# Kernel tuning notes

Hardware: AMD Instinct MI355X
Metric: run time of the kernel (lower is better)

The kernel has to match this reference:

```python
import jax, jax.numpy as jnp
import numpy as np
import math

# BDH config (defaults from BDHConfig)
D = 256        # n_embd
NH = 4         # n_head
MULT = 128     # mlp_internal_dim_multiplier
N = MULT * D // NH   # 8192 latent dim per head
NLAYER = 6
VOCAB = 256
B, T = 1, 1024
THETA = 2.0 ** 16
TWO_PI = 2.0 * math.pi


def _freqs(n):
    # get_freqs: quantize exponent to even integers
    t = jnp.arange(n, dtype=jnp.float32)
    q = jnp.floor(t / 2.0) * 2.0
    return 1.0 / (THETA ** (q / n)) / TWO_PI  # [N]


def _ln(x, eps=1e-5):
    # LayerNorm without affine params (elementwise_affine=False)
    m = jnp.mean(x, axis=-1, keepdims=True)
    v = jnp.mean((x - m) ** 2, axis=-1, keepdims=True)
    return (x - m) / jnp.sqrt(v + eps)


def _rope(phases, v):
    # phases: [T,N] broadcastable to v [...,T,N]
    ph = (phases % 1.0) * TWO_PI
    cos, sin = jnp.cos(ph), jnp.sin(ph)
    # rotate adjacent pairs: (-v_odd, v_even) interleaved
    vrot = jnp.stack((-v[..., 1::2], v[..., ::2]), axis=-1).reshape(v.shape)
    return v * cos + vrot * sin


def setup_inputs() -> dict:
    key = jax.random.key(0)
    ks = jax.random.split(key, 6)
    std = 0.02
    return {
        "idx": jax.random.randint(ks[0], (B, T), 0, VOCAB),
        "embed_w": jax.random.normal(ks[1], (VOCAB, D), jnp.float32) * std,
        "encoder": jax.random.normal(ks[2], (NH, D, N), jnp.float32) * std,
        "encoder_v": jax.random.normal(ks[3], (NH, D, N), jnp.float32) * std,
        "decoder": jax.random.normal(ks[4], (NH * N, D), jnp.float32) * std,
        "lm_head": jax.random.normal(ks[5], (D, VOCAB), jnp.float32) * std,
    }


def reference(idx, embed_w, encoder, encoder_v, decoder, lm_head):
    freqs = _freqs(N)                                             # [N]
    phases = jnp.arange(T, dtype=jnp.float32)[:, None] * freqs    # [T,N]
    mask = jnp.tril(jnp.ones((T, T), jnp.float32), k=-1)          # strict causal
    dec = decoder.reshape(NH, N, D)

    x = _ln(embed_w[idx])                                         # [B,T,D]
    for _ in range(NLAYER):
        x_sp = jax.nn.relu(jnp.einsum('btd,hdn->bhtn', x, encoder))   # [B,nh,T,N]
        qr = _rope(phases, x_sp)                                       # [B,nh,T,N]
        scores = jnp.einsum('bhtn,bhsn->bhts', qr, qr) * mask          # [B,nh,T,T]
        ykv = _ln(jnp.einsum('bhts,bsd->bhtd', scores, x))             # [B,nh,T,D]
        y_sp = jax.nn.relu(jnp.einsum('bhtd,hdn->bhtn', ykv, encoder_v))
        xy = x_sp * y_sp                                               # [B,nh,T,N]
        ymlp = jnp.einsum('bhtn,hnd->btd', xy, dec)                    # [B,T,D]
        x = _ln(x + _ln(ymlp))
    return x @ lm_head                                                 # [B,T,VOCAB]
```

## Files before the change

kernel.cpp:

```cpp
#include <hip/hip_runtime.h>
#include <hip/hip_bf16.h>
#include <math.h>

#define T_ 1024
#define D_ 256
#define N_ 8192
#define NH_ 4
#define NLAYER_ 6
#define VOCAB_ 256
#define TWO_PI_F 6.283185307179586f
#define INV_TWO_PI_F 0.15915494309189535f

#define SC_HSTR32 294912u
#define SC_SSTR32 1179648u
#define SC_SPLIT_BYTES 4718592u
#define SC_NSPLIT 8

typedef __attribute__((ext_vector_type(8))) short short8;
typedef __attribute__((ext_vector_type(4))) float floatx4;
typedef unsigned short ushort_t;

__device__ __forceinline__ void cp16(const void* g, void* l) {
    __builtin_amdgcn_global_load_lds((const __attribute__((address_space(1))) unsigned int*)g,
                                     (__attribute__((address_space(3))) unsigned int*)l,
                                     16, 0, 0);
}

__device__ __forceinline__ float bf2f_raw(unsigned short u) {
    union { unsigned int i; float f; } x;
    x.i = ((unsigned int)u) << 16;
    return x.f;
}
__device__ __forceinline__ unsigned int f2bf_u(float f) {
    union { float f; unsigned int u; } x; x.f = f;
    return (x.u + 0x7fffu + ((x.u >> 16) & 1u)) >> 16;
}
__device__ __forceinline__ float fsin_rev(float ph) {
    float r; asm("v_sin_f32 %0, %1" : "=v"(r) : "v"(ph)); return r;
}
__device__ __forceinline__ float fcos_rev(float ph) {
    float r; asm("v_cos_f32 %0, %1" : "=v"(r) : "v"(ph)); return r;
}

__device__ __forceinline__ float block_sum(float v, float* red) {
    #pragma unroll
    for (int s = 32; s > 0; s >>= 1) v += __shfl_xor(v, s);
    int tid = threadIdx.x;
    if ((tid & 63) == 0) red[tid >> 6] = v;
    __syncthreads();
    float r = red[0] + red[1] + red[2] + red[3];
    __syncthreads();
    return r;
}


__global__ void k_embed_ln(const int* __restrict__ idx, const float* __restrict__ ew,
                           float* __restrict__ x, __hip_bfloat16* __restrict__ x_bf) {
    __shared__ float red[4];
    int t = blockIdx.x, d = threadIdx.x;
    float v = ew[idx[t] * D_ + d];
    float mean = block_sum(v, red) * (1.0f / D_);
    float c = v - mean;
    float var = block_sum(c * c, red) * (1.0f / D_);
    float o = c * rsqrtf(var + 1e-5f);
    x[t * D_ + d] = o;
    x_bf[t * D_ + d] = __float2bfloat16(o);
}

__global__ void k_ln_rows(const float* __restrict__ yp, __hip_bfloat16* __restrict__ outb) {
    __shared__ float red[4];
    int r = blockIdx.x, d = threadIdx.x;
    const size_t S = (size_t)NH_ * T_ * D_;
    float v = yp[(size_t)r * D_ + d] + yp[S + (size_t)r * D_ + d];
    float mean = block_sum(v, red) * (1.0f / D_);
    float c = v - mean;
    float var = block_sum(c * c, red) * (1.0f / D_);
    outb[(size_t)r * D_ + d] = __float2bfloat16(c * rsqrtf(var + 1e-5f));
}

__global__ void k_x_update(float* __restrict__ x, const float* __restrict__ ypart,
                           __hip_bfloat16* __restrict__ x_bf) {
    __shared__ float red[4];
    int t = blockIdx.x, d = threadIdx.x;
    float v = 0.0f;
    #pragma unroll
    for (int i = 0; i < 32; i++) v += ypart[(size_t)i * T_ * D_ + t * D_ + d];
    float m1 = block_sum(v, red) * (1.0f / D_);
    float c1 = v - m1;
    float v1 = block_sum(c1 * c1, red) * (1.0f / D_);
    float u = c1 * rsqrtf(v1 + 1e-5f);
    float w = x[t * D_ + d] + u;
    float m2 = block_sum(w, red) * (1.0f / D_);
    float c2 = w - m2;
    float v2 = block_sum(c2 * c2, red) * (1.0f / D_);
    float o = c2 * rsqrtf(v2 + 1e-5f);
    x[t * D_ + d] = o;
    x_bf[t * D_ + d] = __float2bfloat16(o);
}

__global__ __launch_bounds__(256) void k_tcvt(const float* __restrict__ in,
                                              __hip_bfloat16* __restrict__ out,
                                              int R, int C) {
    int h = blockIdx.z;
    int r0 = blockIdx.y * 32, c0 = blockIdx.x * 32;
    __shared__ float tile[32][33];
    int tx = threadIdx.x & 31, ty = threadIdx.x >> 5;
    const float* inh = in + (size_t)h * R * C;
    __hip_bfloat16* outh = out + (size_t)h * R * C;
    #pragma unroll
    for (int i = 0; i < 4; i++)
        tile[ty + 8 * i][tx] = inh[(size_t)(r0 + ty + 8 * i) * C + c0 + tx];
    __syncthreads();
    #pragma unroll
    for (int i = 0; i < 4; i++)
        outh[(size_t)(c0 + ty + 8 * i) * R + r0 + tx] = __float2bfloat16(tile[tx][ty + 8 * i]);
}

__device__ __forceinline__ void gemm128(const ushort_t* __restrict__ A,
                                        const ushort_t* __restrict__ B,
                                        int lda, int ldb, int K,
                                        ushort_t* As, ushort_t* Bs,
                                        floatx4 acc[4][4]) {
    const int tid = threadIdx.x;
    const int lane = tid & 63, wid = tid >> 6;
    const int wm = wid >> 1, wn = wid & 1;
    const int quad = lane >> 4, col = lane & 15;
    int srow[4], scol[4];
    #pragma unroll
    for (int i = 0; i < 4; i++) {
        int s = i * 256 + tid;
        srow[i] = s >> 3;
        scol[i] = (s & 7) ^ (srow[i] & 7);
    }
    for (int k0 = 0; k0 < K; k0 += 64) {
        #pragma unroll
        for (int i = 0; i < 4; i++)
            cp16(A + (size_t)srow[i] * lda + k0 + scol[i] * 8,
                 As + (size_t)(i * 256 + wid * 64) * 8);
        #pragma unroll
        for (int i = 0; i < 4; i++)
            cp16(B + (size_t)srow[i] * ldb + k0 + scol[i] * 8,
                 Bs + (size_t)(i * 256 + wid * 64) * 8);
        __syncthreads();
        #pragma unroll
        for (int kk = 0; kk < 2; kk++) {
            short8 af[4], bf[4];
            #pragma unroll
            for (int mi = 0; mi < 4; mi++) {
                int row = wm * 64 + mi * 16 + col;
                int pc = ((kk << 2) + quad) ^ (row & 7);
                af[mi] = *(const short8*)&As[row * 64 + pc * 8];
            }
            #pragma unroll
            for (int ni = 0; ni < 4; ni++) {
                int row = wn * 64 + ni * 16 + col;
                int pc = ((kk << 2) + quad) ^ (row & 7);
                bf[ni] = *(const short8*)&Bs[row * 64 + pc * 8];
            }
            #pragma unroll
            for (int mi = 0; mi < 4; mi++)
                #pragma unroll
                for (int ni = 0; ni < 4; ni++)
                    acc[mi][ni] = __builtin_amdgcn_mfma_f32_16x16x32_bf16(
                        af[mi], bf[ni], acc[mi][ni], 0, 0, 0);
        }
        __syncthreads();
    }
}

#define GEMM_PROLOGUE()                                              \
    __shared__ __align__(16) ushort_t smem[2 * 128 * 64];            \
    ushort_t* As = smem;                                             \
    ushort_t* Bs = smem + 128 * 64;                                  \
    floatx4 acc[4][4];                                               \
    _Pragma("unroll") for (int mi = 0; mi < 4; mi++)                 \
        _Pragma("unroll") for (int ni = 0; ni < 4; ni++)             \
            acc[mi][ni] = (floatx4){0.f, 0.f, 0.f, 0.f};             \
    const int lane = threadIdx.x & 63, wid = threadIdx.x >> 6;       \
    const int wm = wid >> 1, wn = wid & 1;                           \
    const int quad = lane >> 4, col = lane & 15;                     \
    const int odd = lane & 1;                                        \
    const int rsel = odd ? 2 : 0, rother = odd ? 0 : 2;

__global__ __launch_bounds__(256) void k_scores_m(const __hip_bfloat16* __restrict__ qr,
                                                  __hip_bfloat16* __restrict__ scp) {
    const int b = blockIdx.x;
    const int slice = b & 31;
    const int h = slice & 3, ks = slice >> 2;
    int i = b >> 5;
    int ti = 0;
    while ((ti + 1) * (ti + 2) / 2 <= i) ti++;
    int si = i - ti * (ti + 1) / 2;
    const int t0 = ti * 128, s0 = si * 128;
    GEMM_PROLOGUE();
    const ushort_t* qh = (const ushort_t*)qr + (size_t)h * T_ * N_ + (size_t)ks * (N_ / 8);
    gemm128(qh + (size_t)t0 * N_, qh + (size_t)s0 * N_, N_, N_, N_ / 8, As, Bs, acc);
    unsigned int* osm = (unsigned int*)smem;
    #pragma unroll
    for (int mi = 0; mi < 4; mi++)
        #pragma unroll
        for (int ni = 0; ni < 4; ni++) {
            const int ss = s0 + wn * 64 + ni * 16 + col;
            const int cc = (wn * 64 + ni * 16 + col) >> 1;
            const int rowb = wm * 64 + mi * 16 + quad * 4;
            #pragma unroll
            for (int rr = 0; rr < 2; rr++) {
                int tt_o = rowb + rother + rr;
                float send = (ss < t0 + tt_o) ? acc[mi][ni][rother + rr] : 0.0f;
                float recv = __shfl_xor(send, 1);
                int tt = rowb + rsel + rr;
                float mine = (ss < t0 + tt) ? acc[mi][ni][rsel + rr] : 0.0f;
                float lo = odd ? recv : mine, hi = odd ? mine : recv;
                osm[tt * 64 + (cc ^ ((tt & 7) << 3))] = f2bf_u(lo) | (f2bf_u(hi) << 16);
            }
        }
    __syncthreads();
    const unsigned int Wu = (unsigned int)(ti + 1) * 64;
    unsigned int* bb = (unsigned int*)scp + (size_t)ks * SC_SSTR32 + (size_t)h * SC_HSTR32
                       + (size_t)4096 * ti * (ti + 1);
    uint4* sc4 = (uint4*)bb;
    const uint4* osm4 = (const uint4*)osm;
    #pragma unroll
    for (int i2 = 0; i2 < 8; i2++) {
        int idx = i2 * 256 + threadIdx.x;
        int row = idx >> 4, c4 = idx & 15;
        uint4 w = osm4[row * 16 + (c4 ^ ((row & 7) << 1))];
        sc4[((size_t)row * Wu + (size_t)si * 64) / 4 + c4] = w;
    }
}

__global__ void k_sc_cvt(__hip_bfloat16* __restrict__ scp) {
    const uint4* __restrict__ sp4 = (const uint4*)scp;
    uint4* sp4o = (uint4*)scp;
    int b = blockIdx.x;
    int head = b & 3;
    unsigned int t4 = (unsigned int)(b >> 2) * 256u + threadIdx.x;
    size_t off = (size_t)head * (SC_HSTR32 / 4) + t4;
    float a0 = 0.f, a1 = 0.f, a2 = 0.f, a3 = 0.f, a4 = 0.f, a5 = 0.f, a6 = 0.f, a7 = 0.f;
    #pragma unroll
    for (int s = 0; s < SC_NSPLIT; s++) {
        uint4 w = sp4[off + (size_t)s * (SC_SSTR32 / 4)];
        a0 += bf2f_raw((unsigned short)(w.x & 0xffff));
        a1 += bf2f_raw((unsigned short)(w.x >> 16));
        a2 += bf2f_raw((unsigned short)(w.y & 0xffff));
        a3 += bf2f_raw((unsigned short)(w.y >> 16));
        a4 += bf2f_raw((unsigned short)(w.z & 0xffff));
        a5 += bf2f_raw((unsigned short)(w.z >> 16));
        a6 += bf2f_raw((unsigned short)(w.w & 0xffff));
        a7 += bf2f_raw((unsigned short)(w.w >> 16));
    }
    uint4 o;
    o.x = f2bf_u(a0) | (f2bf_u(a1) << 16);
    o.y = f2bf_u(a2) | (f2bf_u(a3) << 16);
    o.z = f2bf_u(a4) | (f2bf_u(a5) << 16);
    o.w = f2bf_u(a6) | (f2bf_u(a7) << 16);
    sp4o[off] = o;
}

template <int MODE>
__global__ __launch_bounds__(256) void k_proj_m(const __hip_bfloat16* __restrict__ Abf,
                                                const __hip_bfloat16* __restrict__ Wt,
                                                __hip_bfloat16* __restrict__ out1) {
    const int h = blockIdx.z;
    const int t0 = blockIdx.y * 128, n0 = blockIdx.x * 128;
    GEMM_PROLOGUE();
    const ushort_t* Ah = (const ushort_t*)Abf + (MODE ? (size_t)h * T_ * D_ : (size_t)0)
                         + (size_t)t0 * D_;
    const ushort_t* Bh = (const ushort_t*)Wt + (size_t)h * N_ * D_ + (size_t)n0 * D_;
    gemm128(Ah, Bh, D_, D_, D_, As, Bs, acc);
    unsigned int* osm = (unsigned int*)smem;
    unsigned int xw[4][4][2];
    if (MODE == 1) {
        const unsigned int* q32 = (const unsigned int*)out1;
        const int c4p = lane & 15, rl4 = lane >> 4;
        #pragma unroll
        for (int i = 0; i < 8; i++) {
            int chunk = i * 4 + wid;
            int row_l = chunk * 4 + rl4;
            size_t g32 = (size_t)(h * T_ + t0 + row_l) * (size_t)(N_ / 2) + (size_t)(n0 >> 1)
                         + (size_t)(4 * (c4p ^ ((row_l & 7) << 1)));
            cp16(q32 + g32, osm + chunk * 256);
        }
        __syncthreads();
        #pragma unroll
        for (int ni = 0; ni < 4; ni++) {
            const int cc = (wn * 64 + ni * 16 + col) >> 1;
            #pragma unroll
            for (int mi = 0; mi < 4; mi++) {
                const int rowb = wm * 64 + mi * 16 + quad * 4;
                #pragma unroll
                for (int rr = 0; rr < 2; rr++) {
                    int tt = rowb + rsel + rr;
                    xw[ni][mi][rr] = osm[tt * 64 + (cc ^ ((tt & 7) << 3))];
                }
            }
        }
        __syncthreads();
    }
    #pragma unroll
    for (int ni = 0; ni < 4; ni++) {
        const int cc = (wn * 64 + ni * 16 + col) >> 1;
        const int nn_e = (n0 + wn * 64 + ni * 16 + col) & ~1;
        const float freq = exp2f((float)(nn_e >> 1) * (-1.0f / 256.0f)) * INV_TWO_PI_F;
        #pragma unroll
        for (int mi = 0; mi < 4; mi++) {
            const int rowb = wm * 64 + mi * 16 + quad * 4;
            #pragma unroll
            for (int rr = 0; rr < 2; rr++) {
                float send = fmaxf(acc[mi][ni][rother + rr], 0.0f);
                float recv = __shfl_xor(send, 1);
                float mine = fmaxf(acc[mi][ni][rsel + rr], 0.0f);
                float ve = odd ? recv : mine, vo = odd ? mine : recv;
                int tt = rowb + rsel + rr;
                float ph = (float)(t0 + tt) * freq;
                ph -= floorf(ph);
                float c = fcos_rev(ph), s = fsin_rev(ph);
                unsigned int pk;
                if (MODE == 0) {
                    pk = f2bf_u(ve * c - vo * s) | (f2bf_u(vo * c + ve * s) << 16);
                } else {
                    unsigned int w = xw[ni][mi][rr];
                    float qe = bf2f_raw((unsigned short)(w & 0xffff));
                    float qo = bf2f_raw((unsigned short)(w >> 16));
                    pk = f2bf_u(ve * (qe * c + qo * s)) | (f2bf_u(vo * (qo * c - qe * s)) << 16);
                }
                osm[tt * 64 + (cc ^ ((tt & 7) << 3))] = pk;
            }
        }
    }
    __syncthreads();
    uint4* o4 = (uint4*)out1;
    const uint4* osm4 = (const uint4*)osm;
    #pragma unroll
    for (int i2 = 0; i2 < 8; i2++) {
        int idx = i2 * 256 + threadIdx.x;
        int row = idx >> 4, c4 = idx & 15;
        uint4 w = osm4[row * 16 + (c4 ^ ((row & 7) << 1))];
        o4[(size_t)(h * T_ + t0 + row) * (size_t)(N_ / 8) + (size_t)(n0 >> 3) + c4] = w;
    }
}

__global__ __launch_bounds__(256) void k_ykv_m(const __hip_bfloat16* __restrict__ sc,
                                               const __hip_bfloat16* __restrict__ xT,
                                               float* __restrict__ ykvp) {
    const int b = blockIdx.x;
    const int h = (b >> 1) & 3, ks = b & 1;
    const int r0 = b >> 3;
    const int d0 = (r0 & 1) * 128, t0 = (r0 >> 1) * 128;
    GEMM_PROLOGUE();
    const int W = t0 + 128;
    const int half = W >> 1;
    const int ti = t0 >> 7;
    const ushort_t* Ah = (const ushort_t*)sc + (size_t)h * 589824u
                         + (size_t)8192 * ti * (ti + 1) + (size_t)ks * half;
    const ushort_t* Bh = (const ushort_t*)xT + (size_t)d0 * T_ + (size_t)ks * half;
    gemm128(Ah, Bh, W, T_, half, As, Bs, acc);
    float2* yp = (float2*)(ykvp + (size_t)ks * NH_ * T_ * D_);
    #pragma unroll
    for (int mi = 0; mi < 4; mi++)
        #pragma unroll
        for (int ni = 0; ni < 4; ni++) {
            const int dd_e = (d0 + wn * 64 + ni * 16 + col) & ~1;
            const int rowb = t0 + wm * 64 + mi * 16 + quad * 4;
            #pragma unroll
            for (int rr = 0; rr < 2; rr++) {
                float send = acc[mi][ni][rother + rr];
                float recv = __shfl_xor(send, 1);
                float mine = acc[mi][ni][rsel + rr];
                int tt = rowb + rsel + rr;
                yp[(((size_t)h * T_ + tt) * D_ + dd_e) >> 1] =
                    odd ? make_float2(recv, mine) : make_float2(mine, recv);
            }
        }
}

__global__ __launch_bounds__(256) void k_ymlp_m(const __hip_bfloat16* __restrict__ xy,
                                                const __hip_bfloat16* __restrict__ decT,
                                                float* __restrict__ ypart) {
    const int b = blockIdx.x;
    const int slice = b & 31;
    const int ks = slice >> 2, h = slice & 3;
    const int r0 = b >> 5;
    const int d0 = (r0 & 1) * 128, t0 = (r0 >> 1) * 128;
    GEMM_PROLOGUE();
    const ushort_t* Ah = (const ushort_t*)xy + (size_t)h * T_ * N_ + (size_t)t0 * N_ + ks * 1024;
    const ushort_t* Bh = (const ushort_t*)decT + (size_t)h * D_ * N_ + (size_t)d0 * N_ + ks * 1024;
    gemm128(Ah, Bh, N_, N_, 1024, As, Bs, acc);
    float2* yp = (float2*)(ypart + (size_t)slice * T_ * D_);
    #pragma unroll
    for (int mi = 0; mi < 4; mi++)
        #pragma unroll
        for (int ni = 0; ni < 4; ni++) {
            const int dd_e = (d0 + wn * 64 + ni * 16 + col) & ~1;
            const int rowb = t0 + wm * 64 + mi * 16 + quad * 4;
            #pragma unroll
            for (int rr = 0; rr < 2; rr++) {
                float send = acc[mi][ni][rother + rr];
                float recv = __shfl_xor(send, 1);
                float mine = acc[mi][ni][rsel + rr];
                int tt = rowb + rsel + rr;
                yp[((size_t)tt * D_ + dd_e) >> 1] =
                    odd ? make_float2(recv, mine) : make_float2(mine, recv);
            }
        }
}

__global__ __launch_bounds__(256) void k_lmhead_m(const __hip_bfloat16* __restrict__ x_bf,
                                                  const __hip_bfloat16* __restrict__ lmT,
                                                  float* __restrict__ out) {
    const int v0 = blockIdx.x * 128, t0 = blockIdx.y * 128;
    GEMM_PROLOGUE();
    const ushort_t* Ah = (const ushort_t*)x_bf + (size_t)t0 * D_;
    const ushort_t* Bh = (const ushort_t*)lmT + (size_t)v0 * D_;
    gemm128(Ah, Bh, D_, D_, D_, As, Bs, acc);
    float2* op = (float2*)out;
    #pragma unroll
    for (int mi = 0; mi < 4; mi++)
        #pragma unroll
        for (int ni = 0; ni < 4; ni++) {
            const int vv_e = (v0 + wn * 64 + ni * 16 + col) & ~1;
            const int rowb = t0 + wm * 64 + mi * 16 + quad * 4;
            #pragma unroll
            for (int rr = 0; rr < 2; rr++) {
                float send = acc[mi][ni][rother + rr];
                float recv = __shfl_xor(send, 1);
                float mine = acc[mi][ni][rsel + rr];
                int tt = rowb + rsel + rr;
                op[((size_t)tt * VOCAB_ + vv_e) >> 1] =
                    odd ? make_float2(recv, mine) : make_float2(mine, recv);
            }
        }
}


extern "C" void kernel_launch(void* const* d_in, const int* in_sizes, int n_in,
                              void* d_out, int out_size, void* d_ws, size_t ws_size,
                              hipStream_t stream) {
    const int* idx = (const int*)d_in[0];
    const float* embed_w = (const float*)d_in[1];
    const float* encoder = (const float*)d_in[2];
    const float* encoder_v = (const float*)d_in[3];
    const float* decoder = (const float*)d_in[4];
    const float* lm_head = (const float*)d_in[5];
    float* out = (float*)d_out;

    char* p = (char*)d_ws;
    auto alloc = [&](size_t bytes) {
        char* q = p;
        p += (bytes + 255) & ~(size_t)255;
        return q;
    };
    float* x = (float*)alloc((size_t)T_ * D_ * 4);
    __hip_bfloat16* x_bf = (__hip_bfloat16*)alloc((size_t)T_ * D_ * 2);
    __hip_bfloat16* xT = (__hip_bfloat16*)alloc((size_t)T_ * D_ * 2);
    __hip_bfloat16* ykv_bf = (__hip_bfloat16*)alloc((size_t)NH_ * T_ * D_ * 2);
    __hip_bfloat16* scp = (__hip_bfloat16*)alloc((size_t)SC_NSPLIT * SC_SPLIT_BYTES);
    __hip_bfloat16* qr = (__hip_bfloat16*)alloc((size_t)NH_ * T_ * N_ * 2);
    __hip_bfloat16* encT = (__hip_bfloat16*)alloc((size_t)NH_ * N_ * D_ * 2);
    __hip_bfloat16* encvT = (__hip_bfloat16*)alloc((size_t)NH_ * N_ * D_ * 2);
    __hip_bfloat16* decT = (__hip_bfloat16*)alloc((size_t)NH_ * N_ * D_ * 2);
    __hip_bfloat16* lmT = (__hip_bfloat16*)alloc((size_t)VOCAB_ * D_ * 2);
    float* ypart = (float*)alloc((size_t)32 * T_ * D_ * 4);
    float* ykvp = (float*)((char*)scp + SC_SPLIT_BYTES);

    k_tcvt<<<dim3(N_ / 32, D_ / 32, NH_), 256, 0, stream>>>(encoder, encT, D_, N_);
    k_tcvt<<<dim3(N_ / 32, D_ / 32, NH_), 256, 0, stream>>>(encoder_v, encvT, D_, N_);
    k_tcvt<<<dim3(D_ / 32, N_ / 32, NH_), 256, 0, stream>>>(decoder, decT, N_, D_);
    k_tcvt<<<dim3(VOCAB_ / 32, D_ / 32, 1), 256, 0, stream>>>(lm_head, lmT, D_, VOCAB_);

    k_embed_ln<<<T_, 256, 0, stream>>>(idx, embed_w, x, x_bf);
    for (int l = 0; l < NLAYER_; l++) {
        k_proj_m<0><<<dim3(N_ / 128, T_ / 128, NH_), 256, 0, stream>>>(x_bf, encT, qr);
        k_scores_m<<<36 * 32, 256, 0, stream>>>(qr, scp);
        k_sc_cvt<<<1152, 256, 0, stream>>>(scp);
        k_tcvt<<<dim3(D_ / 32, T_ / 32, 1), 256, 0, stream>>>(x, xT, T_, D_);
        k_ykv_m<<<16 * 8, 256, 0, stream>>>(scp, xT, ykvp);
        k_ln_rows<<<NH_ * T_, 256, 0, stream>>>(ykvp, ykv_bf);
        k_proj_m<1><<<dim3(N_ / 128, T_ / 128, NH_), 256, 0, stream>>>(ykv_bf, encvT, qr );
        k_ymlp_m<<<16 * 32, 256, 0, stream>>>(qr, decT, ypart);
        k_x_update<<<T_, 256, 0, stream>>>(x, ypart, x_bf);
    }
    k_lmhead_m<<<dim3(VOCAB_ / 128, T_ / 128), 256, 0, stream>>>(x_bf, lmT, out);
}
```

Before: 1.306 ms.

## Widen projection tiles to 128x256 and split ykv K-range four ways

The projection GEMM now computes a 128x256 output tile per block with its own inline MFMA loop, reusing each loaded A tile across twice as many columns. The RoPE/gating epilogue runs in two 128-column halves. The ykv kernel splits the causal K range into four balanced chunks instead of two, doubling the block count. The row LayerNorm now sums four partial buffers. The trade-off is higher register and LDS pressure in the projection kernel, which may lower occupancy, plus extra partial-sum traffic for ykv.

```diff
diff --git a/kernel.cpp b/kernel.cpp
--- a/kernel.cpp
+++ b/kernel.cpp
@@ -71,7 +71,9 @@
     __shared__ float red[4];
     int r = blockIdx.x, d = threadIdx.x;
     const size_t S = (size_t)NH_ * T_ * D_;
-    float v = yp[(size_t)r * D_ + d] + yp[S + (size_t)r * D_ + d];
+    float v = 0.0f;
+    #pragma unroll
+    for (int s = 0; s < 4; s++) v += yp[(size_t)s * S + (size_t)r * D_ + d];
     float mean = block_sum(v, red) * (1.0f / D_);
     float c = v - mean;
     float var = block_sum(c * c, red) * (1.0f / D_);
@@ -262,81 +264,142 @@
                                                 const __hip_bfloat16* __restrict__ Wt,
                                                 __hip_bfloat16* __restrict__ out1) {
     const int h = blockIdx.z;
-    const int t0 = blockIdx.y * 128, n0 = blockIdx.x * 128;
-    GEMM_PROLOGUE();
+    const int t0 = blockIdx.y * 128, n0 = blockIdx.x * 256;
+    __shared__ __align__(16) ushort_t smem[(128 + 256) * 64];
+    ushort_t* As = smem;
+    ushort_t* Bs = smem + 128 * 64;
+    floatx4 acc[4][8];
+    #pragma unroll
+    for (int mi = 0; mi < 4; mi++)
+        #pragma unroll
+        for (int nj = 0; nj < 8; nj++) acc[mi][nj] = (floatx4){0.f, 0.f, 0.f, 0.f};
+    const int tid = threadIdx.x;
+    const int lane = tid & 63, wid = tid >> 6;
+    const int wm = wid >> 1, wn = wid & 1;
+    const int quad = lane >> 4, col = lane & 15;
+    const int odd = lane & 1;
+    const int rsel = odd ? 2 : 0, rother = odd ? 0 : 2;
     const ushort_t* Ah = (const ushort_t*)Abf + (MODE ? (size_t)h * T_ * D_ : (size_t)0)
                          + (size_t)t0 * D_;
     const ushort_t* Bh = (const ushort_t*)Wt + (size_t)h * N_ * D_ + (size_t)n0 * D_;
-    gemm128(Ah, Bh, D_, D_, D_, As, Bs, acc);
+    int srA[4], scA[4], srB[8], scB[8];
+    #pragma unroll
+    for (int i = 0; i < 4; i++) {
+        int s = i * 256 + tid;
+        srA[i] = s >> 3; scA[i] = (s & 7) ^ (srA[i] & 7);
+    }
+    #pragma unroll
+    for (int i = 0; i < 8; i++) {
+        int s = i * 256 + tid;
+        srB[i] = s >> 3; scB[i] = (s & 7) ^ (srB[i] & 7);
+    }
+    for (int k0 = 0; k0 < D_; k0 += 64) {
+        #pragma unroll
+        for (int i = 0; i < 4; i++)
+            cp16(Ah + (size_t)srA[i] * D_ + k0 + scA[i] * 8, As + (i * 256 + wid * 64) * 8);
+        #pragma unroll
+        for (int i = 0; i < 8; i++)
+            cp16(Bh + (size_t)srB[i] * D_ + k0 + scB[i] * 8, Bs + (i * 256 + wid * 64) * 8);
+        __syncthreads();
+        #pragma unroll
+        for (int kk = 0; kk < 2; kk++) {
+            short8 af[4], bfv[8];
+            #pragma unroll
+            for (int mi = 0; mi < 4; mi++) {
+                int row = wm * 64 + mi * 16 + col;
+                int pc = ((kk << 2) + quad) ^ (row & 7);
+                af[mi] = *(const short8*)&As[row * 64 + pc * 8];
+            }
+            #pragma unroll
+            for (int nj = 0; nj < 8; nj++) {
+                int row = (nj >> 2) * 128 + wn * 64 + (nj & 3) * 16 + col;
+                int pc = ((kk << 2) + quad) ^ (row & 7);
+                bfv[nj] = *(const short8*)&Bs[row * 64 + pc * 8];
+            }
+            #pragma unroll
+            for (int mi = 0; mi < 4; mi++)
+                #pragma unroll
+                for (int nj = 0; nj < 8; nj++)
+                    acc[mi][nj] = __builtin_amdgcn_mfma_f32_16x16x32_bf16(
+                        af[mi], bfv[nj], acc[mi][nj], 0, 0, 0);
+        }
+        __syncthreads();
+    }
     unsigned int* osm = (unsigned int*)smem;
-    unsigned int xw[4][4][2];
-    if (MODE == 1) {
-        const unsigned int* q32 = (const unsigned int*)out1;
-        const int c4p = lane & 15, rl4 = lane >> 4;
-        #pragma unroll
-        for (int i = 0; i < 8; i++) {
-            int chunk = i * 4 + wid;
-            int row_l = chunk * 4 + rl4;
-            size_t g32 = (size_t)(h * T_ + t0 + row_l) * (size_t)(N_ / 2) + (size_t)(n0 >> 1)
-                         + (size_t)(4 * (c4p ^ ((row_l & 7) << 1)));
-            cp16(q32 + g32, osm + chunk * 256);
+    #pragma unroll
+    for (int h2 = 0; h2 < 2; h2++) {
+        unsigned int xw[4][4][2];
+        if (MODE == 1) {
+            const unsigned int* q32 = (const unsigned int*)out1;
+            const int c4p = lane & 15, rl4 = lane >> 4;
+            #pragma unroll
+            for (int i = 0; i < 8; i++) {
+                int chunk = i * 4 + wid;
+                int row_l = chunk * 4 + rl4;
+                size_t g32 = (size_t)(h * T_ + t0 + row_l) * (size_t)(N_ / 2)
+                             + (size_t)((n0 + h2 * 128) >> 1)
+                             + (size_t)(4 * (c4p ^ ((row_l & 7) << 1)));
+                cp16(q32 + g32, osm + chunk * 256);
+            }
+            __syncthreads();
+            #pragma unroll
+            for (int ni = 0; ni < 4; ni++) {
+                const int cc = (wn * 64 + ni * 16 + col) >> 1;
+                #pragma unroll
+                for (int mi = 0; mi < 4; mi++) {
+                    const int rowb = wm * 64 + mi * 16 + quad * 4;
+                    #pragma unroll
+                    for (int rr = 0; rr < 2; rr++) {
+                        int tt = rowb + rsel + rr;
+                        xw[ni][mi][rr] = osm[tt * 64 + (cc ^ ((tt & 7) << 3))];
+                    }
+                }
+            }
         }
         __syncthreads();
         #pragma unroll
         for (int ni = 0; ni < 4; ni++) {
             const int cc = (wn * 64 + ni * 16 + col) >> 1;
+            const int nn_e = (n0 + h2 * 128 + wn * 64 + ni * 16 + col) & ~1;
+            const float freq = exp2f((float)(nn_e >> 1) * (-1.0f / 256.0f)) * INV_TWO_PI_F;
             #pragma unroll
             for (int mi = 0; mi < 4; mi++) {
                 const int rowb = wm * 64 + mi * 16 + quad * 4;
                 #pragma unroll
                 for (int rr = 0; rr < 2; rr++) {
+                    float send = fmaxf(acc[mi][h2 * 4 + ni][rother + rr], 0.0f);
+                    float recv = __shfl_xor(send, 1);
+                    float mine = fmaxf(acc[mi][h2 * 4 + ni][rsel + rr], 0.0f);
+                    float ve = odd ? recv : mine, vo = odd ? mine : recv;
                     int tt = rowb + rsel + rr;
-                    xw[ni][mi][rr] = osm[tt * 64 + (cc ^ ((tt & 7) << 3))];
+                    float ph = (float)(t0 + tt) * freq;
+                    ph -= floorf(ph);
+                    float c = fcos_rev(ph), s = fsin_rev(ph);
+                    unsigned int pk;
+                    if (MODE == 0) {
+                        pk = f2bf_u(ve * c - vo * s) | (f2bf_u(vo * c + ve * s) << 16);
+                    } else {
+                        unsigned int w = xw[ni][mi][rr];
+                        float qe = bf2f_raw((unsigned short)(w & 0xffff));
+                        float qo = bf2f_raw((unsigned short)(w >> 16));
+                        pk = f2bf_u(ve * (qe * c + qo * s)) | (f2bf_u(vo * (qo * c - qe * s)) << 16);
+                    }
+                    osm[tt * 64 + (cc ^ ((tt & 7) << 3))] = pk;
                 }
             }
         }
         __syncthreads();
-    }
-    #pragma unroll
-    for (int ni = 0; ni < 4; ni++) {
-        const int cc = (wn * 64 + ni * 16 + col) >> 1;
-        const int nn_e = (n0 + wn * 64 + ni * 16 + col) & ~1;
-        const float freq = exp2f((float)(nn_e >> 1) * (-1.0f / 256.0f)) * INV_TWO_PI_F;
-        #pragma unroll
-        for (int mi = 0; mi < 4; mi++) {
-            const int rowb = wm * 64 + mi * 16 + quad * 4;
-            #pragma unroll
-            for (int rr = 0; rr < 2; rr++) {
-                float send = fmaxf(acc[mi][ni][rother + rr], 0.0f);
-                float recv = __shfl_xor(send, 1);
-                float mine = fmaxf(acc[mi][ni][rsel + rr], 0.0f);
-                float ve = odd ? recv : mine, vo = odd ? mine : recv;
-                int tt = rowb + rsel + rr;
-                float ph = (float)(t0 + tt) * freq;
-                ph -= floorf(ph);
-                float c = fcos_rev(ph), s = fsin_rev(ph);
-                unsigned int pk;
-                if (MODE == 0) {
-                    pk = f2bf_u(ve * c - vo * s) | (f2bf_u(vo * c + ve * s) << 16);
-                } else {
-                    unsigned int w = xw[ni][mi][rr];
-                    float qe = bf2f_raw((unsigned short)(w & 0xffff));
-                    float qo = bf2f_raw((unsigned short)(w >> 16));
-                    pk = f2bf_u(ve * (qe * c + qo * s)) | (f2bf_u(vo * (qo * c - qe * s)) << 16);
-                }
-                osm[tt * 64 + (cc ^ ((tt & 7) << 3))] = pk;
-            }
-        }
-    }
-    __syncthreads();
-    uint4* o4 = (uint4*)out1;
-    const uint4* osm4 = (const uint4*)osm;
-    #pragma unroll
-    for (int i2 = 0; i2 < 8; i2++) {
-        int idx = i2 * 256 + threadIdx.x;
-        int row = idx >> 4, c4 = idx & 15;
-        uint4 w = osm4[row * 16 + (c4 ^ ((row & 7) << 1))];
-        o4[(size_t)(h * T_ + t0 + row) * (size_t)(N_ / 8) + (size_t)(n0 >> 3) + c4] = w;
+        uint4* o4 = (uint4*)out1;
+        const uint4* osm4 = (const uint4*)osm;
+        #pragma unroll
+        for (int i2 = 0; i2 < 8; i2++) {
+            int idx2 = i2 * 256 + tid;
+            int row = idx2 >> 4, c4 = idx2 & 15;
+            uint4 w = osm4[row * 16 + (c4 ^ ((row & 7) << 1))];
+            o4[(size_t)(h * T_ + t0 + row) * (size_t)(N_ / 8)
+               + (size_t)((n0 + h2 * 128) >> 3) + c4] = w;
+        }
+        __syncthreads();
     }
 }
 
@@ -344,17 +407,21 @@
                                                const __hip_bfloat16* __restrict__ xT,
                                                float* __restrict__ ykvp) {
     const int b = blockIdx.x;
-    const int h = (b >> 1) & 3, ks = b & 1;
-    const int r0 = b >> 3;
+    const int ks = b & 3, h = (b >> 2) & 3;
+    const int r0 = b >> 4;
     const int d0 = (r0 & 1) * 128, t0 = (r0 >> 1) * 128;
     GEMM_PROLOGUE();
     const int W = t0 + 128;
-    const int half = W >> 1;
     const int ti = t0 >> 7;
+    const int nc = W >> 6;
+    const int q = nc >> 2, rmd = nc & 3;
+    const int cnt = q + (ks < rmd ? 1 : 0);
+    const int start = ks * q + (ks < rmd ? ks : rmd);
+    const int K = cnt * 64, koff = start * 64;
     const ushort_t* Ah = (const ushort_t*)sc + (size_t)h * 589824u
-                         + (size_t)8192 * ti * (ti + 1) + (size_t)ks * half;
-    const ushort_t* Bh = (const ushort_t*)xT + (size_t)d0 * T_ + (size_t)ks * half;
-    gemm128(Ah, Bh, W, T_, half, As, Bs, acc);
+                         + (size_t)8192 * ti * (ti + 1) + (size_t)koff;
+    const ushort_t* Bh = (const ushort_t*)xT + (size_t)d0 * T_ + (size_t)koff;
+    gemm128(Ah, Bh, W, T_, K, As, Bs, acc);
     float2* yp = (float2*)(ykvp + (size_t)ks * NH_ * T_ * D_);
     #pragma unroll
     for (int mi = 0; mi < 4; mi++)
@@ -470,13 +537,13 @@
 
     k_embed_ln<<<T_, 256, 0, stream>>>(idx, embed_w, x, x_bf);
     for (int l = 0; l < NLAYER_; l++) {
-        k_proj_m<0><<<dim3(N_ / 128, T_ / 128, NH_), 256, 0, stream>>>(x_bf, encT, qr);
+        k_proj_m<0><<<dim3(N_ / 256, T_ / 128, NH_), 256, 0, stream>>>(x_bf, encT, qr);
         k_scores_m<<<36 * 32, 256, 0, stream>>>(qr, scp);
         k_sc_cvt<<<1152, 256, 0, stream>>>(scp);
         k_tcvt<<<dim3(D_ / 32, T_ / 32, 1), 256, 0, stream>>>(x, xT, T_, D_);
-        k_ykv_m<<<16 * 8, 256, 0, stream>>>(scp, xT, ykvp);
+        k_ykv_m<<<256, 256, 0, stream>>>(scp, xT, ykvp);
         k_ln_rows<<<NH_ * T_, 256, 0, stream>>>(ykvp, ykv_bf);
-        k_proj_m<1><<<dim3(N_ / 128, T_ / 128, NH_), 256, 0, stream>>>(ykv_bf, encvT, qr );
+        k_proj_m<1><<<dim3(N_ / 256, T_ / 128, NH_), 256, 0, stream>>>(ykv_bf, encvT, qr );
         k_ymlp_m<<<16 * 32, 256, 0, stream>>>(qr, decT, ypart);
         k_x_update<<<T_, 256, 0, stream>>>(x, ypart, x_bf);
     }
```

Result: slower. 1.583 ms (+21.2%).
